# Performance work log

Measured on AMD Instinct MI355X. Metric: run time of the kernel, lower is better.

The kernel has to match this reference:

```python
import jax, jax.numpy as jnp
import numpy as np

WINDOW_SIZES = (1, 2, 3)
ALPHA = 0.2          # LeakyReLU negative slope
NEG = -9e15          # mask fill value from the torch code


def _xavier(key, shape, gain=np.sqrt(2.0)):
    fan_in, fan_out = shape[0], shape[1]
    std = gain * np.sqrt(2.0 / (fan_in + fan_out))
    return jax.random.normal(key, shape, jnp.float32) * std


def setup_inputs() -> dict:
    key = jax.random.key(0)
    k1, k2, k3, k4, k5 = jax.random.split(key, 5)
    T, B, D, F = 512, 64, 256, 256  # turns, batch, input_dim, output_dim (must match)
    return {
        "local_semantic_vectors": jax.random.normal(k1, (T, B, D), jnp.float32),
        "input_turns": jax.random.randint(k2, (B,), 0, T),  # turns[bt] <= T-1
        "W": _xavier(k3, (D, F)),
        "a1": _xavier(k4, (F, 1)),
        "a2": _xavier(k5, (F, 1)),
    }


def _window_mean(x, w):
    # x: [B, T, D] -> sliding-window mean over axis 1 (window w), zero-padded at end.
    B, T, D = x.shape
    xp = jnp.pad(x, ((0, 0), (0, w - 1), (0, 0)))
    acc = xp[:, :T]
    for j in range(1, w):  # w <= 3, tiny unrolled loop
        acc = acc + xp[:, j:j + T]
    return acc / w


def reference(local_semantic_vectors, input_turns, W, a1, a2):
    # local_semantic_vectors: [T, B, D] -> [B, T, D]
    x = jnp.swapaxes(local_semantic_vectors, 0, 1)
    B, T, D = x.shape
    t_idx = jnp.arange(T)

    num = jnp.zeros((B, W.shape[1]), jnp.float32)
    vws = jnp.zeros((B,), jnp.float32)  # number of window sizes with cnt > 0

    for w in WINDOW_SIZES:
        # number of valid windows per sample: t runs while w+t-1 <= turns
        cnt = jnp.maximum(input_turns - w + 2, 0)                  # [B]
        valid = t_idx[None, :] < cnt[:, None]                      # [B, T]

        # pooled window vectors, zero beyond cnt (max_turn padded to T;
        # padded rows are fully masked and dropped, so the result matches)
        pooled = jnp.where(valid[:, :, None], _window_mean(x, w), 0.0)  # [B, T, D]

        # GAT-style masked self-attention
        h = pooled @ W                                             # [B, T, F]
        f1 = h @ a1                                                # [B, T, 1]
        f2 = h @ a2                                                # [B, T, 1]
        e = jax.nn.leaky_relu(f1 + jnp.swapaxes(f2, 1, 2), ALPHA)  # [B, T, T]
        mask = valid[:, :, None] & valid[:, None, :]
        attn = jax.nn.softmax(jnp.where(mask, e, NEG), axis=-1)
        h_prime = attn @ h                                         # [B, T, F]

        # mean over the first cnt rows
        denom = jnp.maximum(cnt, 1).astype(jnp.float32)
        inter = (h_prime * valid[:, :, None]).sum(axis=1) / denom[:, None]  # [B, F]

        has = (cnt > 0).astype(jnp.float32)
        num = num + inter * has[:, None]
        vws = vws + has

    # cnt is non-increasing in w, so windows with cnt>0 are exactly the first vws;
    # vws >= 1 always (w=1 gives cnt = turns + 2 >= 2).
    return num / vws[:, None]
```

## Files before the change

kernel.cpp:

```cpp
#include <hip/hip_runtime.h>
#include <math.h>

#define T_DIM 512
#define B_DIM 64
#define D_DIM 256
#define F_DIM 256
#define ALPHA 0.2f
#define L2E 1.44269504089f
#define NEGL -1.0e38f

#define U_OFF 0
#define V_OFF 256
#define P_OFF 512
#define Q_OFF (P_OFF + B_DIM * T_DIM)
#define GG_OFF (Q_OFF + B_DIM * T_DIM)

__device__ __forceinline__ float dot4(float4 a, float4 b) {
    return a.x * b.x + a.y * b.y + a.z * b.z + a.w * b.w;
}

__global__ __launch_bounds__(256) void g_uv(const float* __restrict__ W,
                                            const float* __restrict__ a1,
                                            const float* __restrict__ a2,
                                            float* __restrict__ ws) {
    int tid = threadIdx.x;
    int wave = tid >> 6, lane = tid & 63;
    int d = blockIdx.x * 4 + wave;
    float4 wv = ((const float4*)(W + (size_t)d * F_DIM))[lane];
    float4 a1v = ((const float4*)a1)[lane];
    float4 a2v = ((const float4*)a2)[lane];
    float p = dot4(wv, a1v), q = dot4(wv, a2v);
    for (int off = 32; off > 0; off >>= 1) {
        p += __shfl_down(p, off);
        q += __shfl_down(q, off);
    }
    if (lane == 0) {
        ws[U_OFF + d] = p;
        ws[V_OFF + d] = q;
    }
}

__global__ __launch_bounds__(512) void g_pq(const float* __restrict__ x,
                                            const int* __restrict__ turns,
                                            float* __restrict__ ws) {
    __shared__ float su[D_DIM], sv[D_DIM];
    int tid = threadIdx.x;
    if (tid < 64) ((float4*)su)[tid] = ((const float4*)(ws + U_OFF))[tid];
    else if (tid < 128) ((float4*)sv)[tid - 64] = ((const float4*)(ws + V_OFF))[tid - 64];
    __syncthreads();
    int lane = tid & 63;
    int gw = blockIdx.x * 8 + (tid >> 6);
    int b = gw & 63;
    int tbase = gw >> 6;
    int tn = turns[b];
    float4 uv = ((const float4*)su)[lane];
    float4 vv = ((const float4*)sv)[lane];
    float4 xv[8];
#pragma unroll
    for (int k = 0; k < 8; ++k) {
        int t = min(tbase + k * 64, tn);
        xv[k] = ((const float4*)x)[((size_t)t * B_DIM + b) * (D_DIM / 4) + lane];
    }
#pragma unroll
    for (int k = 0; k < 8; ++k) {
        int t = tbase + k * 64;
        if (t <= tn) {
            float pp = dot4(xv[k], uv), qq = dot4(xv[k], vv);
            for (int off = 32; off > 0; off >>= 1) {
                pp += __shfl_down(pp, off);
                qq += __shfl_down(qq, off);
            }
            if (lane == 0) {
                ws[P_OFF + b * T_DIM + t] = pp;
                ws[Q_OFF + b * T_DIM + t] = qq;
            }
        }
    }
}

__global__ __launch_bounds__(1024) void g_attn(const int* __restrict__ turns,
                                               float* __restrict__ ws,
                                               float* __restrict__ out) {
    int bi = blockIdx.x, tid = threadIdx.x;
    if (bi < 32 && tid < 512) out[bi * 512 + tid] = 0.f;
    int b = bi / 3, w = bi % 3 + 1;
    int tn = turns[b];
    int cnt = tn - w + 2;
    if (cnt > T_DIM) cnt = T_DIM;
    float* GG = ws + GG_OFF + ((w - 1) * B_DIM + b) * T_DIM;
    if (cnt <= 0) {
        if (tid < 512) GG[tid] = 0.f;
        return;
    }
    __shared__ float sp[T_DIM], sq[T_DIM];
    __shared__ float f2L[T_DIM], fx[T_DIM];
    __shared__ float2 fc[T_DIM];
    __shared__ float part[2][T_DIM];
    __shared__ float red[8];

    if (tid < 128) ((float4*)sp)[tid] = ((const float4*)(ws + P_OFF + b * T_DIM))[tid];
    else if (tid < 256) ((float4*)sq)[tid - 128] = ((const float4*)(ws + Q_OFF + b * T_DIM))[tid - 128];
    __syncthreads();

    float scale = L2E / (float)w;
    int wave = tid >> 6, lane = tid & 63;
    if (tid < 512) {
        int j = tid;
        float v = NEGL;
        if (j < cnt) {
            float a = sq[j];
            if (w > 1) a += sq[j + 1];
            if (w > 2) a += sq[j + 2];
            v = a * scale;
        }
        f2L[j] = v;
        float m = v;
        for (int off = 32; off > 0; off >>= 1) m = fmaxf(m, __shfl_down(m, off));
        if (lane == 0) red[wave] = m;
        float f1 = 0.f;
        if (j < cnt) {
            float a = sp[j];
            if (w > 1) a += sp[j + 1];
            if (w > 2) a += sp[j + 2];
            f1 = a * scale;
        }
        fx[j] = f1;
    }
    __syncthreads();
    float M = red[0];
#pragma unroll
    for (int k = 1; k < 8; ++k) M = fmaxf(M, red[k]);

    {
        int i = tid & 511, jh = tid >> 9;
        float r = 0.f;
        if (i < cnt) {
            float f1 = fx[i];
            float s0 = f1 + M;
            float mrow = fmaxf(s0, ALPHA * s0);
            int j0 = jh * 256;
            int j1 = min(j0 + 256, cnt);
            int n4 = (j1 - j0 + 3) >> 2;
            const float4* f2v = (const float4*)(f2L + j0);
            for (int k = 0; k < n4; ++k) {
                float4 f = f2v[k];
                float s0a = f1 + f.x, s0b = f1 + f.y, s0c = f1 + f.z, s0d = f1 + f.w;
                s0a = fmaxf(s0a, ALPHA * s0a); s0b = fmaxf(s0b, ALPHA * s0b);
                s0c = fmaxf(s0c, ALPHA * s0c); s0d = fmaxf(s0d, ALPHA * s0d);
                r += __builtin_amdgcn_exp2f(s0a - mrow) + __builtin_amdgcn_exp2f(s0b - mrow)
                   + __builtin_amdgcn_exp2f(s0c - mrow) + __builtin_amdgcn_exp2f(s0d - mrow);
            }
        }
        part[jh][i] = r;
    }
    __syncthreads();
    if (tid < 512) {
        int i = tid;
        float2 v = make_float2(0.f, 3.0e38f);
        if (i < cnt) {
            float s0 = fx[i] + M;
            float mrow = fmaxf(s0, ALPHA * s0);
            v = make_float2(fx[i], mrow + __builtin_amdgcn_logf(part[0][i] + part[1][i]));
        }
        fc[i] = v;
    }
    __syncthreads();

    {
        int j = tid & 511, ih = tid >> 9;
        float acc = 0.f;
        if (j < cnt) {
            float f2j = f2L[j];
            int i0 = ih * 256;
            int i1 = min(i0 + 256, cnt);
            int n2 = (i1 - i0 + 1) >> 1;
            const float4* fcv = (const float4*)(fc + i0);
            for (int k = 0; k < n2; ++k) {
                float4 f = fcv[k];
                float sa = f.x + f2j, sb = f.z + f2j;
                sa = fmaxf(sa, ALPHA * sa); sb = fmaxf(sb, ALPHA * sb);
                acc += __builtin_amdgcn_exp2f(sa - f.y) + __builtin_amdgcn_exp2f(sb - f.w);
            }
        }
        part[ih][j] = acc;
    }
    __syncthreads();
    if (tid < 512) {
        int j = tid;
        GG[j] = (j < cnt) ? (part[0][j] + part[1][j]) / (float)cnt : 0.f;
    }
}

__global__ __launch_bounds__(512) void g_zout(const float* __restrict__ x,
                                              const int* __restrict__ turns,
                                              const float* __restrict__ W,
                                              const float* __restrict__ ws,
                                              float* __restrict__ out) {
    int b = blockIdx.x >> 2;
    int chunk = blockIdx.x & 3;
    int tn = turns[b];
    int t0 = chunk * 128;
    if (t0 > tn) return;
    int tid = threadIdx.x;
    __shared__ float Cs[128];
    __shared__ float4 zp[512];
    __shared__ float Zs[D_DIM];
    __shared__ float ored[512];
    if (tid < 128) {
        int t = t0 + tid;
        const float* G1 = ws + GG_OFF + (0 * B_DIM + b) * T_DIM;
        const float* G2 = ws + GG_OFF + (1 * B_DIM + b) * T_DIM;
        const float* G3 = ws + GG_OFF + (2 * B_DIM + b) * T_DIM;
        float g2 = G2[t] + (t >= 1 ? G2[t - 1] : 0.f);
        float g3 = G3[t] + (t >= 1 ? G3[t - 1] : 0.f) + (t >= 2 ? G3[t - 2] : 0.f);
        float vws = 1.f + (tn >= 1 ? 1.f : 0.f) + (tn >= 2 ? 1.f : 0.f);
        Cs[tid] = (G1[t] + 0.5f * g2 + (1.0f / 3.0f) * g3) / vws;
    }
    __syncthreads();
    int wave = tid >> 6, lane = tid & 63;
    float4 z = make_float4(0.f, 0.f, 0.f, 0.f);
    {
        size_t base = ((size_t)(t0 + wave * 16) * B_DIM + b) * (D_DIM / 4) + lane;
#pragma unroll 8
        for (int tt = 0; tt < 16; ++tt) {
            float c = Cs[wave * 16 + tt];
            float4 xv = ((const float4*)x)[base + (size_t)tt * (B_DIM * D_DIM / 4)];
            z.x += c * xv.x; z.y += c * xv.y; z.z += c * xv.z; z.w += c * xv.w;
        }
    }
    zp[tid] = z;
    __syncthreads();
    if (tid < 64) {
        float4 a = zp[tid];
#pragma unroll
        for (int k = 1; k < 8; ++k) {
            float4 bb = zp[k * 64 + tid];
            a.x += bb.x; a.y += bb.y; a.z += bb.z; a.w += bb.w;
        }
        ((float4*)Zs)[tid] = a;
    }
    __syncthreads();
    int f = tid & 255, dh = tid >> 8;
    float acc = 0.f;
#pragma unroll 8
    for (int dd = dh * 128; dd < dh * 128 + 128; ++dd)
        acc += Zs[dd] * W[(size_t)dd * F_DIM + f];
    ored[tid] = acc;
    __syncthreads();
    if (tid < 256)
        atomicAdd(&out[b * F_DIM + tid], ored[tid] + ored[tid + 256]);
}

extern "C" void kernel_launch(void* const* d_in, const int* in_sizes, int n_in,
                              void* d_out, int out_size, void* d_ws, size_t ws_size,
                              hipStream_t stream) {
    const float* x = (const float*)d_in[0];
    const int* turns = (const int*)d_in[1];
    const float* W = (const float*)d_in[2];
    const float* a1 = (const float*)d_in[3];
    const float* a2 = (const float*)d_in[4];
    float* out = (float*)d_out;
    float* ws = (float*)d_ws;

    g_uv<<<B_DIM, 256, 0, stream>>>(W, a1, a2, ws);
    g_pq<<<512, 512, 0, stream>>>(x, turns, ws);
    g_attn<<<B_DIM * 3, 1024, 0, stream>>>(turns, ws, out);
    g_zout<<<B_DIM * 4, 512, 0, stream>>>(x, turns, W, ws, out);
}
```

Baseline: 51.20 us.

## Split attention into row-stat kernel and fuse column sums into output kernel

```diff
diff --git a/kernel.cpp b/kernel.cpp
--- a/kernel.cpp
+++ b/kernel.cpp
@@ -13,28 +13,39 @@
 #define V_OFF 256
 #define P_OFF 512
 #define Q_OFF (P_OFF + B_DIM * T_DIM)
-#define GG_OFF (Q_OFF + B_DIM * T_DIM)
+#define FC_OFF (Q_OFF + B_DIM * T_DIM)
 
 __device__ __forceinline__ float dot4(float4 a, float4 b) {
     return a.x * b.x + a.y * b.y + a.z * b.z + a.w * b.w;
+}
+
+__device__ __forceinline__ float dpp_sum(float x) {
+    union { float f; int i; } a, t;
+    a.f = x;
+    t.i = __builtin_amdgcn_update_dpp(0, a.i, 0x111, 0xf, 0xf, true); a.f += t.f;
+    t.i = __builtin_amdgcn_update_dpp(0, a.i, 0x112, 0xf, 0xf, true); a.f += t.f;
+    t.i = __builtin_amdgcn_update_dpp(0, a.i, 0x114, 0xf, 0xf, true); a.f += t.f;
+    t.i = __builtin_amdgcn_update_dpp(0, a.i, 0x118, 0xf, 0xf, true); a.f += t.f;
+    t.i = __builtin_amdgcn_update_dpp(0, a.i, 0x142, 0xf, 0xf, true); a.f += t.f;
+    t.i = __builtin_amdgcn_update_dpp(0, a.i, 0x143, 0xf, 0xf, true); a.f += t.f;
+    return a.f;
 }
 
 __global__ __launch_bounds__(256) void g_uv(const float* __restrict__ W,
                                             const float* __restrict__ a1,
                                             const float* __restrict__ a2,
-                                            float* __restrict__ ws) {
+                                            float* __restrict__ ws,
+                                            float* __restrict__ out) {
     int tid = threadIdx.x;
+    out[blockIdx.x * 256 + tid] = 0.f;
     int wave = tid >> 6, lane = tid & 63;
     int d = blockIdx.x * 4 + wave;
     float4 wv = ((const float4*)(W + (size_t)d * F_DIM))[lane];
     float4 a1v = ((const float4*)a1)[lane];
     float4 a2v = ((const float4*)a2)[lane];
-    float p = dot4(wv, a1v), q = dot4(wv, a2v);
-    for (int off = 32; off > 0; off >>= 1) {
-        p += __shfl_down(p, off);
-        q += __shfl_down(q, off);
-    }
-    if (lane == 0) {
+    float p = dpp_sum(dot4(wv, a1v));
+    float q = dpp_sum(dot4(wv, a2v));
+    if (lane == 63) {
         ws[U_OFF + d] = p;
         ws[V_OFF + d] = q;
     }
@@ -65,12 +76,9 @@
     for (int k = 0; k < 8; ++k) {
         int t = tbase + k * 64;
         if (t <= tn) {
-            float pp = dot4(xv[k], uv), qq = dot4(xv[k], vv);
-            for (int off = 32; off > 0; off >>= 1) {
-                pp += __shfl_down(pp, off);
-                qq += __shfl_down(qq, off);
-            }
-            if (lane == 0) {
+            float pp = dpp_sum(dot4(xv[k], uv));
+            float qq = dpp_sum(dot4(xv[k], vv));
+            if (lane == 63) {
                 ws[P_OFF + b * T_DIM + t] = pp;
                 ws[Q_OFF + b * T_DIM + t] = qq;
             }
@@ -78,30 +86,22 @@
     }
 }
 
-__global__ __launch_bounds__(1024) void g_attn(const int* __restrict__ turns,
-                                               float* __restrict__ ws,
-                                               float* __restrict__ out) {
+__global__ __launch_bounds__(1024) void g_row(const int* __restrict__ turns,
+                                              float* __restrict__ ws) {
     int bi = blockIdx.x, tid = threadIdx.x;
-    if (bi < 32 && tid < 512) out[bi * 512 + tid] = 0.f;
-    int b = bi / 3, w = bi % 3 + 1;
+    int b = bi / 12, rem = bi % 12;
+    int w = (rem >> 2) + 1, ic = rem & 3;
     int tn = turns[b];
     int cnt = tn - w + 2;
     if (cnt > T_DIM) cnt = T_DIM;
-    float* GG = ws + GG_OFF + ((w - 1) * B_DIM + b) * T_DIM;
-    if (cnt <= 0) {
-        if (tid < 512) GG[tid] = 0.f;
-        return;
-    }
-    __shared__ float sp[T_DIM], sq[T_DIM];
-    __shared__ float f2L[T_DIM], fx[T_DIM];
-    __shared__ float2 fc[T_DIM];
-    __shared__ float part[2][T_DIM];
-    __shared__ float red[8];
-
+    float2* FC = (float2*)(ws + FC_OFF) + ((w - 1) * B_DIM + b) * T_DIM;
+    if (cnt <= 0) return;
+    __shared__ float sp[T_DIM], sq[T_DIM], f2L[T_DIM];
+    __shared__ float part[8][128];
+    __shared__ float redm[8];
     if (tid < 128) ((float4*)sp)[tid] = ((const float4*)(ws + P_OFF + b * T_DIM))[tid];
     else if (tid < 256) ((float4*)sq)[tid - 128] = ((const float4*)(ws + Q_OFF + b * T_DIM))[tid - 128];
     __syncthreads();
-
     float scale = L2E / (float)w;
     int wave = tid >> 6, lane = tid & 63;
     if (tid < 512) {
@@ -116,107 +116,159 @@
         f2L[j] = v;
         float m = v;
         for (int off = 32; off > 0; off >>= 1) m = fmaxf(m, __shfl_down(m, off));
-        if (lane == 0) red[wave] = m;
-        float f1 = 0.f;
-        if (j < cnt) {
-            float a = sp[j];
-            if (w > 1) a += sp[j + 1];
-            if (w > 2) a += sp[j + 2];
-            f1 = a * scale;
-        }
-        fx[j] = f1;
-    }
-    __syncthreads();
-    float M = red[0];
-#pragma unroll
-    for (int k = 1; k < 8; ++k) M = fmaxf(M, red[k]);
-
-    {
-        int i = tid & 511, jh = tid >> 9;
-        float r = 0.f;
-        if (i < cnt) {
-            float f1 = fx[i];
+        if (lane == 0) redm[wave] = m;
+    }
+    __syncthreads();
+    float M = redm[0];
+#pragma unroll
+    for (int k = 1; k < 8; ++k) M = fmaxf(M, redm[k]);
+
+    int il = tid & 127, oct = tid >> 7;
+    int i = ic * 128 + il;
+    float r = 0.f;
+    if (i < cnt) {
+        float a = sp[i];
+        if (w > 1) a += sp[i + 1];
+        if (w > 2) a += sp[i + 2];
+        float f1 = a * scale;
+        float s0 = f1 + M;
+        float mrow = fmaxf(s0, ALPHA * s0);
+        const float4* fv = (const float4*)(f2L + oct * 64);
+#pragma unroll 4
+        for (int k = 0; k < 16; ++k) {
+            float4 f = fv[k];
+            float sa = f1 + f.x, sb = f1 + f.y, sc = f1 + f.z, sd = f1 + f.w;
+            sa = fmaxf(sa, ALPHA * sa); sb = fmaxf(sb, ALPHA * sb);
+            sc = fmaxf(sc, ALPHA * sc); sd = fmaxf(sd, ALPHA * sd);
+            r += __builtin_amdgcn_exp2f(sa - mrow) + __builtin_amdgcn_exp2f(sb - mrow)
+               + __builtin_amdgcn_exp2f(sc - mrow) + __builtin_amdgcn_exp2f(sd - mrow);
+        }
+    }
+    part[oct][il] = r;
+    __syncthreads();
+    if (tid < 128) {
+        int i2 = ic * 128 + tid;
+        float2 pr = make_float2(0.f, 3.0e38f);
+        if (i2 < cnt) {
+            float rt = part[0][tid];
+#pragma unroll
+            for (int k = 1; k < 8; ++k) rt += part[k][tid];
+            float a = sp[i2];
+            if (w > 1) a += sp[i2 + 1];
+            if (w > 2) a += sp[i2 + 2];
+            float f1 = a * scale;
             float s0 = f1 + M;
             float mrow = fmaxf(s0, ALPHA * s0);
-            int j0 = jh * 256;
-            int j1 = min(j0 + 256, cnt);
-            int n4 = (j1 - j0 + 3) >> 2;
-            const float4* f2v = (const float4*)(f2L + j0);
-            for (int k = 0; k < n4; ++k) {
-                float4 f = f2v[k];
-                float s0a = f1 + f.x, s0b = f1 + f.y, s0c = f1 + f.z, s0d = f1 + f.w;
-                s0a = fmaxf(s0a, ALPHA * s0a); s0b = fmaxf(s0b, ALPHA * s0b);
-                s0c = fmaxf(s0c, ALPHA * s0c); s0d = fmaxf(s0d, ALPHA * s0d);
-                r += __builtin_amdgcn_exp2f(s0a - mrow) + __builtin_amdgcn_exp2f(s0b - mrow)
-                   + __builtin_amdgcn_exp2f(s0c - mrow) + __builtin_amdgcn_exp2f(s0d - mrow);
-            }
-        }
-        part[jh][i] = r;
-    }
-    __syncthreads();
-    if (tid < 512) {
-        int i = tid;
-        float2 v = make_float2(0.f, 3.0e38f);
-        if (i < cnt) {
-            float s0 = fx[i] + M;
-            float mrow = fmaxf(s0, ALPHA * s0);
-            v = make_float2(fx[i], mrow + __builtin_amdgcn_logf(part[0][i] + part[1][i]));
-        }
-        fc[i] = v;
-    }
-    __syncthreads();
-
-    {
-        int j = tid & 511, ih = tid >> 9;
-        float acc = 0.f;
-        if (j < cnt) {
-            float f2j = f2L[j];
-            int i0 = ih * 256;
-            int i1 = min(i0 + 256, cnt);
-            int n2 = (i1 - i0 + 1) >> 1;
-            const float4* fcv = (const float4*)(fc + i0);
-            for (int k = 0; k < n2; ++k) {
-                float4 f = fcv[k];
-                float sa = f.x + f2j, sb = f.z + f2j;
-                sa = fmaxf(sa, ALPHA * sa); sb = fmaxf(sb, ALPHA * sb);
-                acc += __builtin_amdgcn_exp2f(sa - f.y) + __builtin_amdgcn_exp2f(sb - f.w);
-            }
-        }
-        part[ih][j] = acc;
-    }
-    __syncthreads();
-    if (tid < 512) {
-        int j = tid;
-        GG[j] = (j < cnt) ? (part[0][j] + part[1][j]) / (float)cnt : 0.f;
-    }
-}
-
-__global__ __launch_bounds__(512) void g_zout(const float* __restrict__ x,
-                                              const int* __restrict__ turns,
-                                              const float* __restrict__ W,
-                                              const float* __restrict__ ws,
-                                              float* __restrict__ out) {
-    int b = blockIdx.x >> 2;
-    int chunk = blockIdx.x & 3;
+            pr = make_float2(f1, mrow + __builtin_amdgcn_logf(rt));
+        }
+        FC[i2] = pr;
+    }
+}
+
+__global__ __launch_bounds__(512) void g_colzout(const float* __restrict__ x,
+                                                 const int* __restrict__ turns,
+                                                 const float* __restrict__ W,
+                                                 const float* __restrict__ ws,
+                                                 float* __restrict__ out) {
+    int b = blockIdx.x >> 2, chunk = blockIdx.x & 3;
     int tn = turns[b];
     int t0 = chunk * 128;
     if (t0 > tn) return;
     int tid = threadIdx.x;
+    __shared__ float sq[T_DIM];
+    __shared__ float4 fcs4[3][T_DIM / 2];
+    __shared__ float Gs[3][132];
+    __shared__ float partq[128][4];
+    __shared__ float part2[2][128];
     __shared__ float Cs[128];
     __shared__ float4 zp[512];
     __shared__ float Zs[D_DIM];
     __shared__ float ored[512];
+
+    if (tid < 128) ((float4*)sq)[tid] = ((const float4*)(ws + Q_OFF + b * T_DIM))[tid];
+    for (int k = tid; k < 3 * 256; k += 512) {
+        int wi = k >> 8, kk = k & 255;
+        fcs4[wi][kk] = ((const float4*)(ws + FC_OFF))[(wi * B_DIM + b) * 256 + kk];
+    }
+    __syncthreads();
+
+    for (int w = 1; w <= 3; ++w) {
+        int cw = tn - w + 2;
+        if (cw > T_DIM) cw = T_DIM;
+        bool act = cw > 0;
+        float scale = L2E / (float)w;
+        if (act) {
+            {
+                int jj = tid >> 2, iq = tid & 3;
+                int j = t0 + jj;
+                float acc = 0.f;
+                if (j < cw) {
+                    float a = sq[j];
+                    if (w > 1) a += sq[j + 1];
+                    if (w > 2) a += sq[j + 2];
+                    float f2j = a * scale;
+                    const float4* fv = fcs4[w - 1] + iq * 64;
+                    for (int k = 0; k < 64; ++k) {
+                        float4 f = fv[k];
+                        float sa = f.x + f2j, sb = f.z + f2j;
+                        sa = fmaxf(sa, ALPHA * sa); sb = fmaxf(sb, ALPHA * sb);
+                        acc += __builtin_amdgcn_exp2f(sa - f.y)
+                             + __builtin_amdgcn_exp2f(sb - f.w);
+                    }
+                }
+                partq[jj][iq] = acc;
+            }
+            if (tid < 256) {
+                int e = tid >> 7, q2 = tid & 127;
+                int j2 = t0 - 2 + e;
+                float acc = 0.f;
+                if (j2 >= 0 && j2 < cw) {
+                    float a = sq[j2];
+                    if (w > 1) a += sq[j2 + 1];
+                    if (w > 2) a += sq[j2 + 2];
+                    float f2j = a * scale;
+                    const float4* fv = fcs4[w - 1] + q2 * 2;
+#pragma unroll
+                    for (int k = 0; k < 2; ++k) {
+                        float4 f = fv[k];
+                        float sa = f.x + f2j, sb = f.z + f2j;
+                        sa = fmaxf(sa, ALPHA * sa); sb = fmaxf(sb, ALPHA * sb);
+                        acc += __builtin_amdgcn_exp2f(sa - f.y)
+                             + __builtin_amdgcn_exp2f(sb - f.w);
+                    }
+                }
+                part2[e][q2] = acc;
+            }
+        }
+        __syncthreads();
+        if (act) {
+            float invc = 1.0f / (float)cw;
+            if (tid < 128) {
+                int j = t0 + tid;
+                float s = partq[tid][0] + partq[tid][1] + partq[tid][2] + partq[tid][3];
+                Gs[w - 1][2 + tid] = (j < cw) ? s * invc : 0.f;
+            } else if (tid < 130) {
+                int e = tid - 128;
+                int j2 = t0 - 2 + e;
+                float s = 0.f;
+                for (int k = 0; k < 128; ++k) s += part2[e][k];
+                Gs[w - 1][e] = (j2 >= 0 && j2 < cw) ? s * invc : 0.f;
+            }
+        } else if (tid < 132) {
+            Gs[w - 1][tid] = 0.f;
+        }
+        __syncthreads();
+    }
+
     if (tid < 128) {
-        int t = t0 + tid;
-        const float* G1 = ws + GG_OFF + (0 * B_DIM + b) * T_DIM;
-        const float* G2 = ws + GG_OFF + (1 * B_DIM + b) * T_DIM;
-        const float* G3 = ws + GG_OFF + (2 * B_DIM + b) * T_DIM;
-        float g2 = G2[t] + (t >= 1 ? G2[t - 1] : 0.f);
-        float g3 = G3[t] + (t >= 1 ? G3[t - 1] : 0.f) + (t >= 2 ? G3[t - 2] : 0.f);
+        float g1 = Gs[0][2 + tid];
+        float g2 = Gs[1][2 + tid] + Gs[1][1 + tid];
+        float g3 = Gs[2][2 + tid] + Gs[2][1 + tid] + Gs[2][tid];
         float vws = 1.f + (tn >= 1 ? 1.f : 0.f) + (tn >= 2 ? 1.f : 0.f);
-        Cs[tid] = (G1[t] + 0.5f * g2 + (1.0f / 3.0f) * g3) / vws;
-    }
-    __syncthreads();
+        Cs[tid] = (g1 + 0.5f * g2 + (1.0f / 3.0f) * g3) / vws;
+    }
+    __syncthreads();
+
     int wave = tid >> 6, lane = tid & 63;
     float4 z = make_float4(0.f, 0.f, 0.f, 0.f);
     {
@@ -262,8 +314,8 @@
     float* out = (float*)d_out;
     float* ws = (float*)d_ws;
 
-    g_uv<<<B_DIM, 256, 0, stream>>>(W, a1, a2, ws);
+    g_uv<<<B_DIM, 256, 0, stream>>>(W, a1, a2, ws, out);
     g_pq<<<512, 512, 0, stream>>>(x, turns, ws);
-    g_attn<<<B_DIM * 3, 1024, 0, stream>>>(turns, ws, out);
-    g_zout<<<B_DIM * 4, 512, 0, stream>>>(x, turns, W, ws, out);
-}
+    g_row<<<B_DIM * 12, 1024, 0, stream>>>(turns, ws);
+    g_colzout<<<B_DIM * 4, 512, 0, stream>>>(x, turns, W, ws, out);
+}
```

New measurement: 47.00 us, median of 2. 1.09x faster.
